# Kernel tuning notes

Hardware: AMD Instinct MI355X
Metric: run time of the kernel (lower is better)

Reference implementation:

```python
import jax, jax.numpy as jnp
import numpy as np

N = 100000
E = 1600000
F_IN = 64
DIM = 64
OUT = 2
BN_EPS = 1e-5


def setup_inputs() -> dict:
    key = jax.random.key(0)
    ks = jax.random.split(key, 12)
    s = lambda fan_in: 1.0 / np.sqrt(fan_in)
    inp = {
        "x": jax.random.normal(ks[0], (N, F_IN), dtype=jnp.float32),
        "edge_index": jax.random.randint(ks[1], (2, E), 0, N, dtype=jnp.int64),
        # conv1 MLP: Linear(F_IN, DIM) -> ReLU -> Linear(DIM, DIM)
        "W1a": jax.random.uniform(ks[2], (F_IN, DIM), jnp.float32, -s(F_IN), s(F_IN)),
        "b1a": jnp.zeros((DIM,), jnp.float32),
        "W1b": jax.random.uniform(ks[3], (DIM, DIM), jnp.float32, -s(DIM), s(DIM)),
        "b1b": jnp.zeros((DIM,), jnp.float32),
        "g1": jnp.ones((DIM,), jnp.float32),
        "be1": jnp.zeros((DIM,), jnp.float32),
        # conv5 MLP: Linear(DIM, DIM) -> ReLU -> Linear(DIM, 2)
        "W5a": jax.random.uniform(ks[4], (DIM, DIM), jnp.float32, -s(DIM), s(DIM)),
        "b5a": jnp.zeros((DIM,), jnp.float32),
        "W5b": jax.random.uniform(ks[5], (DIM, OUT), jnp.float32, -s(DIM), s(DIM)),
        "b5b": jnp.zeros((OUT,), jnp.float32),
        "g5": jnp.ones((OUT,), jnp.float32),
        "be5": jnp.zeros((OUT,), jnp.float32),
    }
    return inp


def _gin_agg(x, src, dst):
    # GINConv with eps=0: (1+eps)*x + sum_{j in N(i)} x_j
    agg = jax.ops.segment_sum(x[src], dst, num_segments=N)
    return x + agg


def _batchnorm(h, gamma, beta):
    mu = jnp.mean(h, axis=0)
    var = jnp.var(h, axis=0)  # biased, as torch BN uses for normalization
    return (h - mu) * jax.lax.rsqrt(var + BN_EPS) * gamma + beta


def reference(x, edge_index, W1a, b1a, W1b, b1b, g1, be1,
              W5a, b5a, W5b, b5b, g5, be5):
    src, dst = edge_index[0], edge_index[1]
    # conv1
    h = _gin_agg(x, src, dst)                      # [N, F_IN]
    h = jax.nn.relu(h @ W1a + b1a) @ W1b + b1b     # [N, DIM]
    h = jax.nn.relu(h)
    h = _batchnorm(h, g1, be1)
    # conv5
    h = _gin_agg(h, src, dst)                      # [N, DIM]
    h = jax.nn.relu(h @ W5a + b5a) @ W5b + b5b     # [N, OUT]
    h = jax.nn.relu(h)
    h = _batchnorm(h, g5, be5)
    return h
```

## Files before the change

### kernel.cpp

```cpp
#include <hip/hip_runtime.h>

#define NN 100000
#define FD 64
#define OUTF 2
#define NB 391
#define P1CH 4096
#define NTILE 6250

typedef short bf16x8 __attribute__((ext_vector_type(8), may_alias));
typedef float f32x4 __attribute__((ext_vector_type(4)));

__device__ inline ushort f2bf(float f) {
    uint u = __float_as_uint(f);
    uint r = (u + 0x7FFFu + ((u >> 16) & 1u)) >> 16;
    return (ushort)r;
}
__device__ inline float bf2f(ushort v) {
    return __uint_as_float(((uint)v) << 16);
}


__global__ void k_zero(float* __restrict__ p, int n) {
    int i = blockIdx.x * blockDim.x + threadIdx.x;
    if (i < n) p[i] = 0.f;
}

__global__ void k_zero2(int* __restrict__ a, int na, float* __restrict__ b, int nb) {
    int i = blockIdx.x * blockDim.x + threadIdx.x;
    if (i < na) a[i] = 0;
    if (i < nb) b[i] = 0.f;
}

__global__ void k_copy4(const float4* __restrict__ s, float4* __restrict__ d, int n4) {
    int i = blockIdx.x * blockDim.x + threadIdx.x;
    int st = gridDim.x * blockDim.x;
    for (; i < n4; i += st) d[i] = s[i];
}

__global__ void k_cvt(const float4* __restrict__ x4, ushort4* __restrict__ xb4, int n4) {
    int i = blockIdx.x * blockDim.x + threadIdx.x;
    int st = gridDim.x * blockDim.x;
    for (; i < n4; i += st) {
        float4 v = x4[i];
        ushort4 w;
        w.x = f2bf(v.x);
        w.y = f2bf(v.y);
        w.z = f2bf(v.z);
        w.w = f2bf(v.w);
        xb4[i] = w;
    }
}


__global__ __launch_bounds__(256) void k_p1a(const int* __restrict__ ei,
                                             int* __restrict__ gcnt, int E_) {
    __shared__ int h[NB];
    int tid = threadIdx.x;
    for (int i = tid; i < NB; i += 256) h[i] = 0;
    __syncthreads();
    int c0 = blockIdx.x * P1CH;
    int c1 = min(c0 + P1CH, E_);
    for (int i = c0 + tid; i < c1; i += 256) {
        int d = ei[E_ + i];
        int b = min(max(d >> 8, 0), NB - 1);
        atomicAdd(&h[b], 1);
    }
    __syncthreads();
    for (int i = tid; i < NB; i += 256) {
        int c = h[i];
        if (c) atomicAdd(&gcnt[i], c);
    }
}

__global__ __launch_bounds__(512) void k_p1scan(const int* __restrict__ gcnt,
                                                int* __restrict__ bbase,
                                                int* __restrict__ bcur) {
    __shared__ int ts[512];
    int tid = threadIdx.x;
    int v = (tid < NB) ? gcnt[tid] : 0;
    ts[tid] = v;
    __syncthreads();
    for (int off = 1; off < 512; off <<= 1) {
        int u = (tid >= off) ? ts[tid - off] : 0;
        __syncthreads();
        ts[tid] += u;
        __syncthreads();
    }
    int excl = ts[tid] - v;
    if (tid < NB) {
        bbase[tid] = excl;
        bcur[tid] = excl;
    }
    if (tid == 511) bbase[NB] = ts[511];
}

__global__ __launch_bounds__(256) void k_p1b(const int* __restrict__ ei,
                                             int* __restrict__ bcur,
                                             int* __restrict__ part, int E_) {
    __shared__ int h[NB];
    __shared__ int base[NB];
    int tid = threadIdx.x;
    for (int i = tid; i < NB; i += 256) h[i] = 0;
    __syncthreads();
    int c0 = blockIdx.x * P1CH;
    int c1 = min(c0 + P1CH, E_);
    for (int i = c0 + tid; i < c1; i += 256) {
        int d = ei[E_ + i];
        int b = min(max(d >> 8, 0), NB - 1);
        atomicAdd(&h[b], 1);
    }
    __syncthreads();
    for (int i = tid; i < NB; i += 256) {
        int c = h[i];
        base[i] = c ? atomicAdd(&bcur[i], c) : 0;
        h[i] = 0;
    }
    __syncthreads();
    for (int i = c0 + tid; i < c1; i += 256) {
        int s = ei[i];
        int d = ei[E_ + i];
        int b = min(max(d >> 8, 0), NB - 1);
        int slot = base[b] + atomicAdd(&h[b], 1);
        part[slot] = ((d & 255) << 20) | (s & 0xFFFFF);
    }
}

__global__ __launch_bounds__(256) void k_build(const int* __restrict__ part,
                                               const int* __restrict__ bbase,
                                               int* __restrict__ rowptr,
                                               int* __restrict__ csr, int E_) {
    __shared__ int cnt[256];
    __shared__ int ts[256];
    __shared__ int cur[256];
    int b = blockIdx.x;
    int tid = threadIdx.x;
    cnt[tid] = 0;
    __syncthreads();
    int s0 = bbase[b], s1 = bbase[b + 1];
    for (int i = s0 + tid; i < s1; i += 256) {
        int v = part[i];
        atomicAdd(&cnt[(v >> 20) & 255], 1);
    }
    __syncthreads();
    int v = cnt[tid];
    ts[tid] = v;
    __syncthreads();
    for (int off = 1; off < 256; off <<= 1) {
        int u = (tid >= off) ? ts[tid - off] : 0;
        __syncthreads();
        ts[tid] += u;
        __syncthreads();
    }
    int excl = ts[tid] - v;
    int node = b * 256 + tid;
    if (node < NN) rowptr[node] = s0 + excl;
    cur[tid] = s0 + excl;
    if (b == 0 && tid == 0) rowptr[NN] = E_;
    __syncthreads();
    for (int i = s0 + tid; i < s1; i += 256) {
        int v2 = part[i];
        int lj = (v2 >> 20) & 255;
        int pos = atomicAdd(&cur[lj], 1);
        csr[pos] = v2 & 0xFFFFF;
    }
}


#define GSTEP(T, A0, A1, A2, A3)                                               \
    {                                                                          \
        int j = (T) * 4 + g;                                                   \
        int s = __shfl(id, j);                                                 \
        float m = (j < cnt) ? 1.f : 0.f;                                       \
        uint2 v = *(const uint2*)(Xb + (long)s * FD + (l << 2));               \
        A0 = fmaf(m, __uint_as_float(v.x << 16), A0);                          \
        A1 = fmaf(m, __uint_as_float(v.x & 0xFFFF0000u), A1);                  \
        A2 = fmaf(m, __uint_as_float(v.y << 16), A2);                          \
        A3 = fmaf(m, __uint_as_float(v.y & 0xFFFF0000u), A3);                  \
    }

__global__ __launch_bounds__(256) void k_gather2(
        const ushort* __restrict__ Xb, const int* __restrict__ rowptr,
        const int* __restrict__ csr, const float4* __restrict__ sc4,
        const float4* __restrict__ sh4, ushort* __restrict__ outb,
        int E_, int affine) {
    int tid = threadIdx.x;
    int lane = tid & 63;
    int n = (blockIdx.x * blockDim.x + tid) >> 6;
    if (n >= NN) return;
    int g = lane >> 4;
    int l = lane & 15;
    int start = rowptr[n], end = rowptr[n + 1];
    start = min(max(start, 0), E_);
    end = min(max(end, start), E_);
    int deg = end - start;

    float a0 = 0.f, a1 = 0.f, a2 = 0.f, a3 = 0.f;
    float b0 = 0.f, b1 = 0.f, b2 = 0.f, b3 = 0.f;
    if (g == 0) {
        uint2 v = *(const uint2*)(Xb + (long)n * FD + (l << 2));
        a0 = __uint_as_float(v.x << 16);
        a1 = __uint_as_float(v.x & 0xFFFF0000u);
        a2 = __uint_as_float(v.y << 16);
        a3 = __uint_as_float(v.y & 0xFFFF0000u);
    }

    for (int base = start; base < end; base += 64) {
        int cnt = min(end - base, 64);
        int id = 0;
        if (lane < cnt) id = min(max(csr[base + lane], 0), NN - 1);
        int nsteps = (cnt + 3) >> 2;
        int t = 0;
        for (; t + 4 <= nsteps; t += 4) {
            GSTEP(t + 0, a0, a1, a2, a3)
            GSTEP(t + 1, b0, b1, b2, b3)
            GSTEP(t + 2, a0, a1, a2, a3)
            GSTEP(t + 3, b0, b1, b2, b3)
        }
        for (; t + 2 <= nsteps; t += 2) {
            GSTEP(t + 0, a0, a1, a2, a3)
            GSTEP(t + 1, b0, b1, b2, b3)
        }
        if (t < nsteps) GSTEP(t, a0, a1, a2, a3)
    }
    a0 += b0; a1 += b1; a2 += b2; a3 += b3;
    a0 += __shfl_xor(a0, 16); a0 += __shfl_xor(a0, 32);
    a1 += __shfl_xor(a1, 16); a1 += __shfl_xor(a1, 32);
    a2 += __shfl_xor(a2, 16); a2 += __shfl_xor(a2, 32);
    a3 += __shfl_xor(a3, 16); a3 += __shfl_xor(a3, 32);

    if (affine) {
        float4 s = sc4[l];
        float4 h = sh4[l];
        float dp1 = (float)(deg + 1);
        a0 = fmaf(a0, s.x, dp1 * h.x);
        a1 = fmaf(a1, s.y, dp1 * h.y);
        a2 = fmaf(a2, s.z, dp1 * h.z);
        a3 = fmaf(a3, s.w, dp1 * h.w);
    }
    if (g == 0) {
        ushort4 v;
        v.x = f2bf(a0); v.y = f2bf(a1); v.z = f2bf(a2); v.w = f2bf(a3);
        ((ushort4*)(outb + (long)n * FD))[l] = v;
    }
}


__global__ __launch_bounds__(256) void k_mlp1_mfma(
        const ushort* __restrict__ Ab,
        const float* __restrict__ Wa, const float* __restrict__ ba,
        const float* __restrict__ Wb, const float* __restrict__ bb,
        ushort* __restrict__ H, float* __restrict__ gsum, float* __restrict__ gsq) {
    __shared__ __attribute__((aligned(16))) short tile[4][16 * 72];
    __shared__ float sArr[64], qArr[64];
    int tid = threadIdx.x;
    int w = tid >> 6, lane = tid & 63;
    int l = lane & 15, quad = lane >> 4;
    if (tid < 64) { sArr[tid] = 0.f; qArr[tid] = 0.f; }
    __syncthreads();

    bf16x8 B1[2][4], B2[2][4];
#pragma unroll
    for (int ks = 0; ks < 2; ks++)
#pragma unroll
        for (int t = 0; t < 4; t++) {
            bf16x8 f1, f2;
#pragma unroll
            for (int j = 0; j < 8; j++) {
                int k = ks * 32 + quad * 8 + j;
                f1[j] = (short)f2bf(Wa[k * 64 + t * 16 + l]);
                f2[j] = (short)f2bf(Wb[k * 64 + t * 16 + l]);
            }
            B1[ks][t] = f1;
            B2[ks][t] = f2;
        }
    float bias1[4], bias2[4];
#pragma unroll
    for (int t = 0; t < 4; t++) {
        bias1[t] = ba[t * 16 + l];
        bias2[t] = bb[t * 16 + l];
    }

    float s[4] = {0.f, 0.f, 0.f, 0.f}, q[4] = {0.f, 0.f, 0.f, 0.f};
    short* tp = &tile[w][0];
    int gw = blockIdx.x * 4 + w;
    int nw = gridDim.x * 4;
    for (int tau = gw; tau < NTILE; tau += nw) {
        int m0 = tau * 16;
        bf16x8 A0 = *(const bf16x8*)(Ab + (size_t)(m0 + l) * FD + quad * 8);
        bf16x8 A1 = *(const bf16x8*)(Ab + (size_t)(m0 + l) * FD + 32 + quad * 8);
#pragma unroll
        for (int t = 0; t < 4; t++) {
            f32x4 c = {0.f, 0.f, 0.f, 0.f};
            c = __builtin_amdgcn_mfma_f32_16x16x32_bf16(A0, B1[0][t], c, 0, 0, 0);
            c = __builtin_amdgcn_mfma_f32_16x16x32_bf16(A1, B1[1][t], c, 0, 0, 0);
#pragma unroll
            for (int r = 0; r < 4; r++) {
                float v = fmaxf(c[r] + bias1[t], 0.f);
                tp[(quad * 4 + r) * 72 + t * 16 + l] = (short)f2bf(v);
            }
        }
        bf16x8 A20 = *(const bf16x8*)&tp[l * 72 + quad * 8];
        bf16x8 A21 = *(const bf16x8*)&tp[l * 72 + 32 + quad * 8];
#pragma unroll
        for (int t = 0; t < 4; t++) {
            f32x4 c = {0.f, 0.f, 0.f, 0.f};
            c = __builtin_amdgcn_mfma_f32_16x16x32_bf16(A20, B2[0][t], c, 0, 0, 0);
            c = __builtin_amdgcn_mfma_f32_16x16x32_bf16(A21, B2[1][t], c, 0, 0, 0);
#pragma unroll
            for (int r = 0; r < 4; r++) {
                float v = fmaxf(c[r] + bias2[t], 0.f);
                s[t] += v;
                q[t] += v * v;
                tp[(quad * 4 + r) * 72 + t * 16 + l] = (short)f2bf(v);
            }
        }
        int row = lane >> 2, ch = lane & 3;
        bf16x8 o0 = *(const bf16x8*)&tp[row * 72 + ch * 16];
        bf16x8 o1 = *(const bf16x8*)&tp[row * 72 + ch * 16 + 8];
        *(bf16x8*)(H + (size_t)(m0 + row) * FD + ch * 16) = o0;
        *(bf16x8*)(H + (size_t)(m0 + row) * FD + ch * 16 + 8) = o1;
    }
#pragma unroll
    for (int t = 0; t < 4; t++) {
        s[t] += __shfl_xor(s[t], 16); s[t] += __shfl_xor(s[t], 32);
        q[t] += __shfl_xor(q[t], 16); q[t] += __shfl_xor(q[t], 32);
    }
    if (quad == 0) {
#pragma unroll
        for (int t = 0; t < 4; t++) {
            atomicAdd(&sArr[t * 16 + l], s[t]);
            atomicAdd(&qArr[t * 16 + l], q[t]);
        }
    }
    __syncthreads();
    if (tid < 64) {
        atomicAdd(&gsum[tid], sArr[tid]);
        atomicAdd(&gsq[tid], qArr[tid]);
    }
}

__global__ __launch_bounds__(256) void k_mlp2_mfma(
        const ushort* __restrict__ Ab,
        const float* __restrict__ Wa, const float* __restrict__ ba,
        const float* __restrict__ Wb2, const float* __restrict__ bb2,
        float* __restrict__ O, float* __restrict__ gsum, float* __restrict__ gsq) {
    __shared__ __attribute__((aligned(16))) short tile[4][16 * 72];
    __shared__ float sArr[2], qArr[2];
    int tid = threadIdx.x;
    int w = tid >> 6, lane = tid & 63;
    int l = lane & 15, quad = lane >> 4;
    if (tid < 2) { sArr[tid] = 0.f; qArr[tid] = 0.f; }
    __syncthreads();

    bf16x8 B1[2][4], B2[2];
#pragma unroll
    for (int ks = 0; ks < 2; ks++) {
#pragma unroll
        for (int t = 0; t < 4; t++) {
            bf16x8 f1;
#pragma unroll
            for (int j = 0; j < 8; j++) {
                int k = ks * 32 + quad * 8 + j;
                f1[j] = (short)f2bf(Wa[k * 64 + t * 16 + l]);
            }
            B1[ks][t] = f1;
        }
        bf16x8 f2;
#pragma unroll
        for (int j = 0; j < 8; j++) {
            int k = ks * 32 + quad * 8 + j;
            f2[j] = (l < OUTF) ? (short)f2bf(Wb2[k * OUTF + l]) : (short)0;
        }
        B2[ks] = f2;
    }
    float bias1[4];
#pragma unroll
    for (int t = 0; t < 4; t++) bias1[t] = ba[t * 16 + l];
    float bias2 = (l < OUTF) ? bb2[l] : 0.f;

    float s = 0.f, q = 0.f;
    short* tp = &tile[w][0];
    int gw = blockIdx.x * 4 + w;
    int nw = gridDim.x * 4;
    for (int tau = gw; tau < NTILE; tau += nw) {
        int m0 = tau * 16;
        bf16x8 A0 = *(const bf16x8*)(Ab + (size_t)(m0 + l) * FD + quad * 8);
        bf16x8 A1 = *(const bf16x8*)(Ab + (size_t)(m0 + l) * FD + 32 + quad * 8);
#pragma unroll
        for (int t = 0; t < 4; t++) {
            f32x4 c = {0.f, 0.f, 0.f, 0.f};
            c = __builtin_amdgcn_mfma_f32_16x16x32_bf16(A0, B1[0][t], c, 0, 0, 0);
            c = __builtin_amdgcn_mfma_f32_16x16x32_bf16(A1, B1[1][t], c, 0, 0, 0);
#pragma unroll
            for (int r = 0; r < 4; r++) {
                float v = fmaxf(c[r] + bias1[t], 0.f);
                tp[(quad * 4 + r) * 72 + t * 16 + l] = (short)f2bf(v);
            }
        }
        bf16x8 A20 = *(const bf16x8*)&tp[l * 72 + quad * 8];
        bf16x8 A21 = *(const bf16x8*)&tp[l * 72 + 32 + quad * 8];
        f32x4 c = {0.f, 0.f, 0.f, 0.f};
        c = __builtin_amdgcn_mfma_f32_16x16x32_bf16(A20, B2[0], c, 0, 0, 0);
        c = __builtin_amdgcn_mfma_f32_16x16x32_bf16(A21, B2[1], c, 0, 0, 0);
#pragma unroll
        for (int r = 0; r < 4; r++) {
            float v = fmaxf(c[r] + bias2, 0.f);
            if (l < OUTF) {
                s += v;
                q += v * v;
                O[(size_t)(m0 + quad * 4 + r) * OUTF + l] = v;
            }
        }
    }
    s += __shfl_xor(s, 16); s += __shfl_xor(s, 32);
    q += __shfl_xor(q, 16); q += __shfl_xor(q, 32);
    if (quad == 0 && l < OUTF) {
        atomicAdd(&sArr[l], s);
        atomicAdd(&qArr[l], q);
    }
    __syncthreads();
    if (tid < OUTF) {
        atomicAdd(&gsum[tid], sArr[tid]);
        atomicAdd(&gsq[tid], qArr[tid]);
    }
}

template <bool BF16OUT>
__global__ __launch_bounds__(256) void k_mlp64(
        const float* __restrict__ X,
        const float* __restrict__ Wa, const float* __restrict__ ba,
        const float* __restrict__ Wb, const float* __restrict__ bb,
        void* __restrict__ Hv, float* __restrict__ gsum, float* __restrict__ gsq) {
    __shared__ float row[256 * 65];
    int tid = threadIdx.x;
    long node = (long)blockIdx.x * 256 + tid;
    bool valid = node < NN;
    if (valid) {
        const float4* rp = (const float4*)(X + node * FD);
#pragma unroll
        for (int q = 0; q < 16; q++) {
            float4 v = rp[q];
            row[tid * 65 + 4 * q + 0] = v.x;
            row[tid * 65 + 4 * q + 1] = v.y;
            row[tid * 65 + 4 * q + 2] = v.z;
            row[tid * 65 + 4 * q + 3] = v.w;
        }
    }
    float acc[64];
#pragma unroll
    for (int j = 0; j < 64; j++) acc[j] = ba[j];
    if (valid) {
        for (int k = 0; k < 64; k++) {
            float xv = row[tid * 65 + k];
            const float* wr = Wa + k * 64;
#pragma unroll
            for (int j = 0; j < 64; j++) acc[j] = fmaf(xv, wr[j], acc[j]);
        }
    }
#pragma unroll
    for (int j = 0; j < 64; j++) row[tid * 65 + j] = fmaxf(acc[j], 0.f);
#pragma unroll
    for (int j = 0; j < 64; j++) acc[j] = bb[j];
    if (valid) {
        for (int k = 0; k < 64; k++) {
            float xv = row[tid * 65 + k];
            const float* wr = Wb + k * 64;
#pragma unroll
            for (int j = 0; j < 64; j++) acc[j] = fmaf(xv, wr[j], acc[j]);
        }
    }
#pragma unroll
    for (int j = 0; j < 64; j++) {
        float v = valid ? fmaxf(acc[j], 0.f) : 0.f;
        row[tid * 65 + j] = v;
    }
    if (valid) {
        if (BF16OUT) {
            ushort4* op = (ushort4*)((ushort*)Hv + node * FD);
#pragma unroll
            for (int q = 0; q < 16; q++) {
                ushort4 w;
                w.x = f2bf(row[tid * 65 + 4 * q + 0]);
                w.y = f2bf(row[tid * 65 + 4 * q + 1]);
                w.z = f2bf(row[tid * 65 + 4 * q + 2]);
                w.w = f2bf(row[tid * 65 + 4 * q + 3]);
                op[q] = w;
            }
        } else {
            float4* op = (float4*)((float*)Hv + node * FD);
#pragma unroll
            for (int q = 0; q < 16; q++) {
                float4 v;
                v.x = row[tid * 65 + 4 * q + 0];
                v.y = row[tid * 65 + 4 * q + 1];
                v.z = row[tid * 65 + 4 * q + 2];
                v.w = row[tid * 65 + 4 * q + 3];
                op[q] = v;
            }
        }
    }
    __syncthreads();
    if (tid < 64) {
        float s = 0.f, q = 0.f;
        for (int r = 0; r < 256; r++) {
            float v = row[r * 65 + tid];
            s += v;
            q += v * v;
        }
        atomicAdd(&gsum[tid], s);
        atomicAdd(&gsq[tid], q);
    }
}

__global__ __launch_bounds__(256) void k_mlp_out(
        const float* __restrict__ X,
        const float* __restrict__ Wa, const float* __restrict__ ba,
        const float* __restrict__ Wb, const float* __restrict__ bb,
        float* __restrict__ O, float* __restrict__ gsum, float* __restrict__ gsq) {
    __shared__ float row[256 * 65];
    __shared__ float red[256][4];
    int tid = threadIdx.x;
    long node = (long)blockIdx.x * 256 + tid;
    bool valid = node < NN;
    if (valid) {
        const float4* rp = (const float4*)(X + node * FD);
#pragma unroll
        for (int q = 0; q < 16; q++) {
            float4 v = rp[q];
            row[tid * 65 + 4 * q + 0] = v.x;
            row[tid * 65 + 4 * q + 1] = v.y;
            row[tid * 65 + 4 * q + 2] = v.z;
            row[tid * 65 + 4 * q + 3] = v.w;
        }
    }
    float acc[64];
#pragma unroll
    for (int j = 0; j < 64; j++) acc[j] = ba[j];
    if (valid) {
        for (int k = 0; k < 64; k++) {
            float xv = row[tid * 65 + k];
            const float* wr = Wa + k * 64;
#pragma unroll
            for (int j = 0; j < 64; j++) acc[j] = fmaf(xv, wr[j], acc[j]);
        }
    }
#pragma unroll
    for (int j = 0; j < 64; j++) row[tid * 65 + j] = fmaxf(acc[j], 0.f);
    float a0 = bb[0];
    float a1 = bb[1];
    if (valid) {
        for (int k = 0; k < 64; k++) {
            float xv = row[tid * 65 + k];
            a0 = fmaf(xv, Wb[k * 2 + 0], a0);
            a1 = fmaf(xv, Wb[k * 2 + 1], a1);
        }
    }
    float v0 = valid ? fmaxf(a0, 0.f) : 0.f;
    float v1 = valid ? fmaxf(a1, 0.f) : 0.f;
    if (valid) {
        float2 v;
        v.x = v0;
        v.y = v1;
        ((float2*)O)[node] = v;
    }
    red[tid][0] = v0;
    red[tid][1] = v0 * v0;
    red[tid][2] = v1;
    red[tid][3] = v1 * v1;
    __syncthreads();
    for (int off = 128; off > 0; off >>= 1) {
        if (tid < off) {
#pragma unroll
            for (int c = 0; c < 4; c++) red[tid][c] += red[tid + off][c];
        }
        __syncthreads();
    }
    if (tid == 0) {
        atomicAdd(&gsum[0], red[0][0]);
        atomicAdd(&gsq[0], red[0][1]);
        atomicAdd(&gsum[1], red[0][2]);
        atomicAdd(&gsq[1], red[0][3]);
    }
}


__global__ void k_bnfin(const float* __restrict__ gsum, const float* __restrict__ gsq,
                        const float* __restrict__ g, const float* __restrict__ be,
                        float* __restrict__ sc, float* __restrict__ sh, int C, float invN) {
    int c = threadIdx.x;
    if (c < C) {
        float mu = gsum[c] * invN;
        float var = gsq[c] * invN - mu * mu;
        float s = g[c] * rsqrtf(var + 1e-5f);
        sc[c] = s;
        sh[c] = fmaf(-mu, s, be[c]);
    }
}

__global__ void k_bn_apply2(float* __restrict__ o, const float* __restrict__ sc,
                            const float* __restrict__ sh, int n) {
    int i = blockIdx.x * blockDim.x + threadIdx.x;
    if (i < n) {
        int c = i & 1;
        o[i] = fmaf(o[i], sc[c], sh[c]);
    }
}


__global__ void k_scatter(const float* __restrict__ x, const int* __restrict__ ei,
                          float* __restrict__ agg, int E_) {
    int lane = threadIdx.x & 63;
    int wid = (blockIdx.x * blockDim.x + threadIdx.x) >> 6;
    int nw = (gridDim.x * blockDim.x) >> 6;
    for (long e = wid; e < E_; e += nw) {
        int s = ei[e];
        int d = ei[E_ + e];
        float v = x[(long)s * FD + lane];
        atomicAdd(&agg[(long)d * FD + lane], v);
    }
}

__global__ void k_scatter_bn(const float* __restrict__ h, const int* __restrict__ ei,
                             const float* __restrict__ sc, const float* __restrict__ sh,
                             float* __restrict__ agg, int E_) {
    int lane = threadIdx.x & 63;
    float scl = sc[lane];
    float shf = sh[lane];
    int wid = (blockIdx.x * blockDim.x + threadIdx.x) >> 6;
    int nw = (gridDim.x * blockDim.x) >> 6;
    for (long e = wid; e < E_; e += nw) {
        int s = ei[e];
        int d = ei[E_ + e];
        float v = fmaf(h[(long)s * FD + lane], scl, shf);
        atomicAdd(&agg[(long)d * FD + lane], v);
    }
}

__global__ void k_bn_copy(const float4* __restrict__ h, const float4* __restrict__ sc4,
                          const float4* __restrict__ sh4, float4* __restrict__ o, int n4) {
    int i = blockIdx.x * blockDim.x + threadIdx.x;
    int st = gridDim.x * blockDim.x;
    for (; i < n4; i += st) {
        float4 v = h[i];
        int c = i & 15;
        float4 s = sc4[c];
        float4 b = sh4[c];
        v.x = fmaf(v.x, s.x, b.x);
        v.y = fmaf(v.y, s.y, b.y);
        v.z = fmaf(v.z, s.z, b.z);
        v.w = fmaf(v.w, s.w, b.w);
        o[i] = v;
    }
}


extern "C" void kernel_launch(void* const* d_in, const int* in_sizes, int n_in,
                              void* d_out, int out_size, void* d_ws, size_t ws_size,
                              hipStream_t stream) {
    const float* x   = (const float*)d_in[0];
    const int*   ei  = (const int*)d_in[1];
    const float* W1a = (const float*)d_in[2];
    const float* b1a = (const float*)d_in[3];
    const float* W1b = (const float*)d_in[4];
    const float* b1b = (const float*)d_in[5];
    const float* g1  = (const float*)d_in[6];
    const float* be1 = (const float*)d_in[7];
    const float* W5a = (const float*)d_in[8];
    const float* b5a = (const float*)d_in[9];
    const float* W5b = (const float*)d_in[10];
    const float* b5b = (const float*)d_in[11];
    const float* g5  = (const float*)d_in[12];
    const float* be5 = (const float*)d_in[13];
    float* out = (float*)d_out;

    const int E = in_sizes[1] / 2;

    float* ws = (float*)d_ws;
    float* agg = ws;
    ushort* aggb = (ushort*)ws;
    ushort* xb  = (ushort*)(ws + 6400000);
    ushort* h1b = (ushort*)(ws + 9600000);
    float* h1_fb = ws + 6400000;
    float* S   = ws + 12800000;
    float* gsum1  = S;
    float* gsq1   = S + 64;
    float* gsum2  = S + 128;
    float* gsq2   = S + 160;
    float* scale1 = S + 192;
    float* shift1 = S + 256;
    float* scale2 = S + 320;
    float* shift2 = S + 328;

    int* ibase  = (int*)(S + 512);
    int* rowptr = ibase;
    int* csr    = ibase + 100004;
    int* gcnt   = ibase + 100004 + E;
    int* bbase  = gcnt + 392;
    int* bcur   = bbase + 396;
    int* part   = (int*)agg;

    size_t needed = (size_t)(12800000 + 512) * 4 + (size_t)(100004 + E + 392 + 396 + 396) * 4;

    const int n4 = NN * FD / 4;
    const int np1 = (E + P1CH - 1) / P1CH;
    const int nblk = (NN + 255) / 256;

    if (ws_size >= needed) {
        k_zero2<<<2, 256, 0, stream>>>(gcnt, NB, S, 192);
        k_cvt<<<2048, 256, 0, stream>>>((const float4*)x, (ushort4*)xb, n4);
        k_p1a<<<np1, 256, 0, stream>>>(ei, gcnt, E);
        k_p1scan<<<1, 512, 0, stream>>>(gcnt, bbase, bcur);
        k_p1b<<<np1, 256, 0, stream>>>(ei, bcur, part, E);
        k_build<<<NB, 256, 0, stream>>>(part, bbase, rowptr, csr, E);

        k_gather2<<<25000, 256, 0, stream>>>(xb, rowptr, csr, nullptr, nullptr, aggb, E, 0);
        k_mlp1_mfma<<<782, 256, 0, stream>>>(aggb, W1a, b1a, W1b, b1b, h1b, gsum1, gsq1);
        k_bnfin<<<1, 64, 0, stream>>>(gsum1, gsq1, g1, be1, scale1, shift1, 64, 1.f / NN);
        k_gather2<<<25000, 256, 0, stream>>>(h1b, rowptr, csr, (const float4*)scale1,
                                             (const float4*)shift1, aggb, E, 1);
        k_mlp2_mfma<<<782, 256, 0, stream>>>(aggb, W5a, b5a, W5b, b5b, out, gsum2, gsq2);
        k_bnfin<<<1, 64, 0, stream>>>(gsum2, gsq2, g5, be5, scale2, shift2, OUTF, 1.f / NN);
        k_bn_apply2<<<(NN * OUTF + 255) / 256, 256, 0, stream>>>(out, scale2, shift2, NN * OUTF);
    } else {
        k_zero<<<1, 256, 0, stream>>>(S, 192);
        k_copy4<<<4096, 256, 0, stream>>>((const float4*)x, (float4*)agg, n4);
        k_scatter<<<4096, 256, 0, stream>>>(x, ei, agg, E);
        k_mlp64<false><<<nblk, 256, 0, stream>>>(agg, W1a, b1a, W1b, b1b,
                                                 (void*)h1_fb, gsum1, gsq1);
        k_bnfin<<<1, 64, 0, stream>>>(gsum1, gsq1, g1, be1, scale1, shift1, 64, 1.f / NN);
        k_bn_copy<<<4096, 256, 0, stream>>>((const float4*)h1_fb, (const float4*)scale1,
                                            (const float4*)shift1, (float4*)agg, n4);
        k_scatter_bn<<<4096, 256, 0, stream>>>(h1_fb, ei, scale1, shift1, agg, E);
        k_mlp_out<<<nblk, 256, 0, stream>>>(agg, W5a, b5a, W5b, b5b, out, gsum2, gsq2);
        k_bnfin<<<1, 64, 0, stream>>>(gsum2, gsq2, g5, be5, scale2, shift2, OUTF, 1.f / NN);
        k_bn_apply2<<<(NN * OUTF + 255) / 256, 256, 0, stream>>>(out, scale2, shift2, NN * OUTF);
    }
}
```

Before: 287.5 us.

## Use per-block histogram scan for edge partition and widen gather loads to 16B

The edge bucketing now stores each block's histogram and runs a column-wise scan, so blocks get deterministic offsets without global atomics and the second pass no longer recounts. The first BN finalize is folded into the second gather, which computes scale and shift per channel. The gather now uses 8 lanes per row with 16-byte loads and 8 neighbors in flight per step, cutting shuffle and load instruction counts. The costs are an extra scan launch, the per-block histogram buffer, and redundant rsqrt math in every gather wave.

```diff
diff --git a/kernel.cpp b/kernel.cpp
--- a/kernel.cpp
+++ b/kernel.cpp
@@ -4,6 +4,7 @@
 #define FD 64
 #define OUTF 2
 #define NB 391
+#define NBP 392
 #define P1CH 4096
 #define NTILE 6250
 
@@ -23,12 +24,6 @@
 __global__ void k_zero(float* __restrict__ p, int n) {
     int i = blockIdx.x * blockDim.x + threadIdx.x;
     if (i < n) p[i] = 0.f;
-}
-
-__global__ void k_zero2(int* __restrict__ a, int na, float* __restrict__ b, int nb) {
-    int i = blockIdx.x * blockDim.x + threadIdx.x;
-    if (i < na) a[i] = 0;
-    if (i < nb) b[i] = 0.f;
 }
 
 __global__ void k_copy4(const float4* __restrict__ s, float4* __restrict__ d, int n4) {
@@ -52,8 +47,8 @@
 }
 
 
-__global__ __launch_bounds__(256) void k_p1a(const int* __restrict__ ei,
-                                             int* __restrict__ gcnt, int E_) {
+__global__ __launch_bounds__(256) void k_p1a2(const int* __restrict__ ei,
+                                              int* __restrict__ ghist, int E_) {
     __shared__ int h[NB];
     int tid = threadIdx.x;
     for (int i = tid; i < NB; i += 256) h[i] = 0;
@@ -66,18 +61,16 @@
         atomicAdd(&h[b], 1);
     }
     __syncthreads();
-    for (int i = tid; i < NB; i += 256) {
-        int c = h[i];
-        if (c) atomicAdd(&gcnt[i], c);
-    }
-}
-
-__global__ __launch_bounds__(512) void k_p1scan(const int* __restrict__ gcnt,
-                                                int* __restrict__ bbase,
-                                                int* __restrict__ bcur) {
+    int* row = ghist + (size_t)blockIdx.x * NBP;
+    for (int i = tid; i < NB; i += 256) row[i] = h[i];
+}
+
+__global__ __launch_bounds__(512) void k_scanCol(int* __restrict__ ghist,
+                                                 int* __restrict__ tot, int np1) {
     __shared__ int ts[512];
-    int tid = threadIdx.x;
-    int v = (tid < NB) ? gcnt[tid] : 0;
+    int b = blockIdx.x;
+    int tid = threadIdx.x;
+    int v = (tid < np1) ? ghist[(size_t)tid * NBP + b] : 0;
     ts[tid] = v;
     __syncthreads();
     for (int off = 1; off < 512; off <<= 1) {
@@ -86,41 +79,45 @@
         ts[tid] += u;
         __syncthreads();
     }
-    int excl = ts[tid] - v;
-    if (tid < NB) {
-        bbase[tid] = excl;
-        bcur[tid] = excl;
-    }
+    if (tid < np1) ghist[(size_t)tid * NBP + b] = ts[tid] - v;
+    if (tid == 511) tot[b] = ts[511];
+}
+
+__global__ __launch_bounds__(512) void k_scanB2(const int* __restrict__ tot,
+                                                int* __restrict__ bbase,
+                                                float* __restrict__ S) {
+    __shared__ int ts[512];
+    int tid = threadIdx.x;
+    if (tid < 192) S[tid] = 0.f;
+    int v = (tid < NB) ? tot[tid] : 0;
+    ts[tid] = v;
+    __syncthreads();
+    for (int off = 1; off < 512; off <<= 1) {
+        int u = (tid >= off) ? ts[tid - off] : 0;
+        __syncthreads();
+        ts[tid] += u;
+        __syncthreads();
+    }
+    if (tid < NB) bbase[tid] = ts[tid] - v;
     if (tid == 511) bbase[NB] = ts[511];
 }
 
-__global__ __launch_bounds__(256) void k_p1b(const int* __restrict__ ei,
-                                             int* __restrict__ bcur,
-                                             int* __restrict__ part, int E_) {
-    __shared__ int h[NB];
-    __shared__ int base[NB];
-    int tid = threadIdx.x;
-    for (int i = tid; i < NB; i += 256) h[i] = 0;
+__global__ __launch_bounds__(256) void k_p1b2(const int* __restrict__ ei,
+                                              const int* __restrict__ ghist,
+                                              const int* __restrict__ bbase,
+                                              int* __restrict__ part, int E_) {
+    __shared__ int cur[NB];
+    int tid = threadIdx.x;
+    const int* row = ghist + (size_t)blockIdx.x * NBP;
+    for (int i = tid; i < NB; i += 256) cur[i] = bbase[i] + row[i];
     __syncthreads();
     int c0 = blockIdx.x * P1CH;
     int c1 = min(c0 + P1CH, E_);
-    for (int i = c0 + tid; i < c1; i += 256) {
-        int d = ei[E_ + i];
-        int b = min(max(d >> 8, 0), NB - 1);
-        atomicAdd(&h[b], 1);
-    }
-    __syncthreads();
-    for (int i = tid; i < NB; i += 256) {
-        int c = h[i];
-        base[i] = c ? atomicAdd(&bcur[i], c) : 0;
-        h[i] = 0;
-    }
-    __syncthreads();
     for (int i = c0 + tid; i < c1; i += 256) {
         int s = ei[i];
         int d = ei[E_ + i];
         int b = min(max(d >> 8, 0), NB - 1);
-        int slot = base[b] + atomicAdd(&h[b], 1);
+        int slot = atomicAdd(&cur[b], 1);
         part[slot] = ((d & 255) << 20) | (s & 0xFFFFF);
     }
 }
@@ -166,81 +163,92 @@
 }
 
 
-#define GSTEP(T, A0, A1, A2, A3)                                               \
-    {                                                                          \
-        int j = (T) * 4 + g;                                                   \
-        int s = __shfl(id, j);                                                 \
-        float m = (j < cnt) ? 1.f : 0.f;                                       \
-        uint2 v = *(const uint2*)(Xb + (long)s * FD + (l << 2));               \
-        A0 = fmaf(m, __uint_as_float(v.x << 16), A0);                          \
-        A1 = fmaf(m, __uint_as_float(v.x & 0xFFFF0000u), A1);                  \
-        A2 = fmaf(m, __uint_as_float(v.y << 16), A2);                          \
-        A3 = fmaf(m, __uint_as_float(v.y & 0xFFFF0000u), A3);                  \
-    }
-
-__global__ __launch_bounds__(256) void k_gather2(
+#define G8STEP(T, A)                                                        \
+    {                                                                       \
+        int j = (T) * 8 + g;                                                \
+        int s = __shfl(id, j);                                              \
+        float m = (j < cnt) ? 1.f : 0.f;                                    \
+        uint4 v = *(const uint4*)(Xb + (long)s * FD + (l << 3));            \
+        A[0] = fmaf(m, __uint_as_float(v.x << 16), A[0]);                   \
+        A[1] = fmaf(m, __uint_as_float(v.x & 0xFFFF0000u), A[1]);           \
+        A[2] = fmaf(m, __uint_as_float(v.y << 16), A[2]);                   \
+        A[3] = fmaf(m, __uint_as_float(v.y & 0xFFFF0000u), A[3]);           \
+        A[4] = fmaf(m, __uint_as_float(v.z << 16), A[4]);                   \
+        A[5] = fmaf(m, __uint_as_float(v.z & 0xFFFF0000u), A[5]);           \
+        A[6] = fmaf(m, __uint_as_float(v.w << 16), A[6]);                   \
+        A[7] = fmaf(m, __uint_as_float(v.w & 0xFFFF0000u), A[7]);           \
+    }
+
+__global__ __launch_bounds__(256) void k_gather3(
         const ushort* __restrict__ Xb, const int* __restrict__ rowptr,
-        const int* __restrict__ csr, const float4* __restrict__ sc4,
-        const float4* __restrict__ sh4, ushort* __restrict__ outb,
-        int E_, int affine) {
+        const int* __restrict__ csr,
+        const float* __restrict__ bs, const float* __restrict__ bq,
+        const float* __restrict__ gam, const float* __restrict__ bet,
+        ushort* __restrict__ outb, int E_, int affine) {
     int tid = threadIdx.x;
     int lane = tid & 63;
     int n = (blockIdx.x * blockDim.x + tid) >> 6;
     if (n >= NN) return;
-    int g = lane >> 4;
-    int l = lane & 15;
+    int g = lane >> 3;
+    int l = lane & 7;
     int start = rowptr[n], end = rowptr[n + 1];
     start = min(max(start, 0), E_);
     end = min(max(end, start), E_);
     int deg = end - start;
 
-    float a0 = 0.f, a1 = 0.f, a2 = 0.f, a3 = 0.f;
-    float b0 = 0.f, b1 = 0.f, b2 = 0.f, b3 = 0.f;
+    float A[8] = {0.f, 0.f, 0.f, 0.f, 0.f, 0.f, 0.f, 0.f};
+    float B[8] = {0.f, 0.f, 0.f, 0.f, 0.f, 0.f, 0.f, 0.f};
     if (g == 0) {
-        uint2 v = *(const uint2*)(Xb + (long)n * FD + (l << 2));
-        a0 = __uint_as_float(v.x << 16);
-        a1 = __uint_as_float(v.x & 0xFFFF0000u);
-        a2 = __uint_as_float(v.y << 16);
-        a3 = __uint_as_float(v.y & 0xFFFF0000u);
+        uint4 v = *(const uint4*)(Xb + (long)n * FD + (l << 3));
+        A[0] = __uint_as_float(v.x << 16);
+        A[1] = __uint_as_float(v.x & 0xFFFF0000u);
+        A[2] = __uint_as_float(v.y << 16);
+        A[3] = __uint_as_float(v.y & 0xFFFF0000u);
+        A[4] = __uint_as_float(v.z << 16);
+        A[5] = __uint_as_float(v.z & 0xFFFF0000u);
+        A[6] = __uint_as_float(v.w << 16);
+        A[7] = __uint_as_float(v.w & 0xFFFF0000u);
     }
 
     for (int base = start; base < end; base += 64) {
         int cnt = min(end - base, 64);
         int id = 0;
         if (lane < cnt) id = min(max(csr[base + lane], 0), NN - 1);
-        int nsteps = (cnt + 3) >> 2;
+        int nsteps = (cnt + 7) >> 3;
         int t = 0;
-        for (; t + 4 <= nsteps; t += 4) {
-            GSTEP(t + 0, a0, a1, a2, a3)
-            GSTEP(t + 1, b0, b1, b2, b3)
-            GSTEP(t + 2, a0, a1, a2, a3)
-            GSTEP(t + 3, b0, b1, b2, b3)
-        }
         for (; t + 2 <= nsteps; t += 2) {
-            GSTEP(t + 0, a0, a1, a2, a3)
-            GSTEP(t + 1, b0, b1, b2, b3)
-        }
-        if (t < nsteps) GSTEP(t, a0, a1, a2, a3)
-    }
-    a0 += b0; a1 += b1; a2 += b2; a3 += b3;
-    a0 += __shfl_xor(a0, 16); a0 += __shfl_xor(a0, 32);
-    a1 += __shfl_xor(a1, 16); a1 += __shfl_xor(a1, 32);
-    a2 += __shfl_xor(a2, 16); a2 += __shfl_xor(a2, 32);
-    a3 += __shfl_xor(a3, 16); a3 += __shfl_xor(a3, 32);
-
-    if (affine) {
-        float4 s = sc4[l];
-        float4 h = sh4[l];
-        float dp1 = (float)(deg + 1);
-        a0 = fmaf(a0, s.x, dp1 * h.x);
-        a1 = fmaf(a1, s.y, dp1 * h.y);
-        a2 = fmaf(a2, s.z, dp1 * h.z);
-        a3 = fmaf(a3, s.w, dp1 * h.w);
+            G8STEP(t, A)
+            G8STEP(t + 1, B)
+        }
+        if (t < nsteps) G8STEP(t, A)
+    }
+#pragma unroll
+    for (int c = 0; c < 8; c++) {
+        float v = A[c] + B[c];
+        v += __shfl_xor(v, 8);
+        v += __shfl_xor(v, 16);
+        v += __shfl_xor(v, 32);
+        A[c] = v;
     }
     if (g == 0) {
-        ushort4 v;
-        v.x = f2bf(a0); v.y = f2bf(a1); v.z = f2bf(a2); v.w = f2bf(a3);
-        ((ushort4*)(outb + (long)n * FD))[l] = v;
+        if (affine) {
+            float dp1 = (float)(deg + 1);
+#pragma unroll
+            for (int c = 0; c < 8; c++) {
+                int ch = l * 8 + c;
+                float mu = bs[ch] * (1.f / NN);
+                float var = bq[ch] * (1.f / NN) - mu * mu;
+                float s = gam[ch] * rsqrtf(var + 1e-5f);
+                float sh = fmaf(-mu, s, bet[ch]);
+                A[c] = fmaf(A[c], s, dp1 * sh);
+            }
+        }
+        uint4 w;
+        w.x = (uint)f2bf(A[0]) | ((uint)f2bf(A[1]) << 16);
+        w.y = (uint)f2bf(A[2]) | ((uint)f2bf(A[3]) << 16);
+        w.z = (uint)f2bf(A[4]) | ((uint)f2bf(A[5]) << 16);
+        w.w = (uint)f2bf(A[6]) | ((uint)f2bf(A[7]) << 16);
+        *(uint4*)(outb + (long)n * FD + (l << 3)) = w;
     }
 }
 
@@ -694,30 +702,31 @@
     int* ibase  = (int*)(S + 512);
     int* rowptr = ibase;
     int* csr    = ibase + 100004;
-    int* gcnt   = ibase + 100004 + E;
-    int* bbase  = gcnt + 392;
-    int* bcur   = bbase + 396;
+    int* bbase  = ibase + 100004 + E;
+    int* tot    = bbase + 400;
+    int* ghist  = tot + 392;
     int* part   = (int*)agg;
 
-    size_t needed = (size_t)(12800000 + 512) * 4 + (size_t)(100004 + E + 392 + 396 + 396) * 4;
+    const int np1 = (E + P1CH - 1) / P1CH;
+    size_t needed = (size_t)(12800000 + 512) * 4 +
+                    (size_t)(100004 + E + 400 + 392 + (size_t)np1 * NBP) * 4;
 
     const int n4 = NN * FD / 4;
-    const int np1 = (E + P1CH - 1) / P1CH;
     const int nblk = (NN + 255) / 256;
 
-    if (ws_size >= needed) {
-        k_zero2<<<2, 256, 0, stream>>>(gcnt, NB, S, 192);
+    if (ws_size >= needed && np1 <= 512) {
         k_cvt<<<2048, 256, 0, stream>>>((const float4*)x, (ushort4*)xb, n4);
-        k_p1a<<<np1, 256, 0, stream>>>(ei, gcnt, E);
-        k_p1scan<<<1, 512, 0, stream>>>(gcnt, bbase, bcur);
-        k_p1b<<<np1, 256, 0, stream>>>(ei, bcur, part, E);
+        k_p1a2<<<np1, 256, 0, stream>>>(ei, ghist, E);
+        k_scanCol<<<NB, 512, 0, stream>>>(ghist, tot, np1);
+        k_scanB2<<<1, 512, 0, stream>>>(tot, bbase, S);
+        k_p1b2<<<np1, 256, 0, stream>>>(ei, ghist, bbase, part, E);
         k_build<<<NB, 256, 0, stream>>>(part, bbase, rowptr, csr, E);
 
-        k_gather2<<<25000, 256, 0, stream>>>(xb, rowptr, csr, nullptr, nullptr, aggb, E, 0);
+        k_gather3<<<25000, 256, 0, stream>>>(xb, rowptr, csr, nullptr, nullptr,
+                                             nullptr, nullptr, aggb, E, 0);
         k_mlp1_mfma<<<782, 256, 0, stream>>>(aggb, W1a, b1a, W1b, b1b, h1b, gsum1, gsq1);
-        k_bnfin<<<1, 64, 0, stream>>>(gsum1, gsq1, g1, be1, scale1, shift1, 64, 1.f / NN);
-        k_gather2<<<25000, 256, 0, stream>>>(h1b, rowptr, csr, (const float4*)scale1,
-                                             (const float4*)shift1, aggb, E, 1);
+        k_gather3<<<25000, 256, 0, stream>>>(h1b, rowptr, csr, gsum1, gsq1,
+                                             g1, be1, aggb, E, 1);
         k_mlp2_mfma<<<782, 256, 0, stream>>>(aggb, W5a, b5a, W5b, b5b, out, gsum2, gsq2);
         k_bnfin<<<1, 64, 0, stream>>>(gsum2, gsq2, g5, be5, scale2, shift2, OUTF, 1.f / NN);
         k_bn_apply2<<<(NN * OUTF + 255) / 256, 256, 0, stream>>>(out, scale2, shift2, NN * OUTF);
```

After: 281.9 us. No clear change (-1.9%).
